# Optimization experiments

Hardware: AMD Instinct MI355X
Metric: run time of the kernel (lower is better)

Reference implementation:

```python
import jax, jax.numpy as jnp
import numpy as np
import math

# static configuration
SPATIAL_SHAPES = [(100, 150), (50, 75), (25, 38), (13, 19)]  # (H, W) per level
EMBED, HEADS, LEVELS, POINTS = 256, 8, 4, 4
HEAD_DIM = EMBED // HEADS
BS = 2
NV = sum(h * w for h, w in SPATIAL_SHAPES)  # 19947
NQ = NV  # encoder-style self-attention (value = query)


def _offset_bias():
    # replicate torch _init_weights grid init for sampling_offsets bias
    thetas = np.arange(HEADS, dtype=np.float32) * (2.0 * math.pi / HEADS)
    grid = np.stack([np.cos(thetas), np.sin(thetas)], -1)  # [H,2]
    grid = grid / np.abs(grid).max(-1, keepdims=True)
    grid = np.tile(grid[:, None, None, :], (1, LEVELS, POINTS, 1))
    for i in range(POINTS):
        grid[:, :, i, :] *= (i + 1)
    return jnp.asarray(grid.reshape(-1), dtype=jnp.float32)


def setup_inputs() -> dict:
    key = jax.random.key(0)
    ks = jax.random.split(key, 8)
    sc = 1.0 / math.sqrt(EMBED)
    return {
        "query": jax.random.normal(ks[0], (BS, NQ, EMBED), jnp.float32),
        "reference_points": jax.random.uniform(ks[1], (BS, NQ, LEVELS, 2), jnp.float32),
        "spatial_shapes": jnp.asarray(SPATIAL_SHAPES, dtype=jnp.int32),
        "W_off": jax.random.normal(ks[2], (EMBED, HEADS * LEVELS * POINTS * 2), jnp.float32) * 0.01,
        "b_off": _offset_bias(),
        "W_attn": jax.random.normal(ks[3], (EMBED, HEADS * LEVELS * POINTS), jnp.float32) * 0.01,
        "b_attn": jnp.zeros((HEADS * LEVELS * POINTS,), jnp.float32),
        "W_val": jax.random.normal(ks[4], (EMBED, EMBED), jnp.float32) * sc,
        "b_val": jnp.zeros((EMBED,), jnp.float32),
        "W_out": jax.random.normal(ks[5], (EMBED, EMBED), jnp.float32) * sc,
        "b_out": jnp.zeros((EMBED,), jnp.float32),
    }


def _bilinear_sample(value_l, loc_l, H, W):
    # value_l: [bs, H*W, heads, hd]; loc_l: [bs, nq, heads, P, 2] normalized coords
    # grid_sample semantics: align_corners=False, padding_mode='zeros'
    x = loc_l[..., 0] * W - 0.5
    y = loc_l[..., 1] * H - 0.5
    x0 = jnp.floor(x)
    y0 = jnp.floor(y)
    dx = x - x0
    dy = y - y0
    x0i = x0.astype(jnp.int32)
    y0i = y0.astype(jnp.int32)

    def gather(xi, yi):
        valid = (xi >= 0) & (xi < W) & (yi >= 0) & (yi < H)  # [bs,nq,h,P]
        idx = jnp.clip(yi, 0, H - 1) * W + jnp.clip(xi, 0, W - 1)
        bs, nq, h, P = idx.shape
        idx2 = idx.transpose(0, 1, 3, 2).reshape(bs, nq * P, h)[..., None]
        v = jnp.take_along_axis(value_l, idx2, axis=1)  # [bs, nq*P, h, hd]
        v = v.reshape(bs, nq, P, h, -1).transpose(0, 1, 3, 2, 4)  # [bs,nq,h,P,hd]
        return v * valid[..., None]

    w00 = ((1 - dx) * (1 - dy))[..., None]
    w01 = (dx * (1 - dy))[..., None]
    w10 = ((1 - dx) * dy)[..., None]
    w11 = (dx * dy)[..., None]
    return (gather(x0i, y0i) * w00 + gather(x0i + 1, y0i) * w01
            + gather(x0i, y0i + 1) * w10 + gather(x0i + 1, y0i + 1) * w11)


def reference(query, reference_points, spatial_shapes, W_off, b_off, W_attn, b_attn,
              W_val, b_val, W_out, b_out):
    bs, nq, _ = query.shape
    # value = query (encoder self-attn), identity = query
    value = (query @ W_val + b_val).reshape(bs, NV, HEADS, HEAD_DIM)
    offs = (query @ W_off + b_off).reshape(bs, nq, HEADS, LEVELS, POINTS, 2)
    attw = jax.nn.softmax((query @ W_attn + b_attn).reshape(bs, nq, HEADS, LEVELS * POINTS), axis=-1)
    attw = attw.reshape(bs, nq, HEADS, LEVELS, POINTS)
    # offset normalizer: (W, H) per level
    norm = jnp.stack([spatial_shapes[:, 1], spatial_shapes[:, 0]], -1).astype(query.dtype)
    loc = reference_points[:, :, None, :, None, :] + offs / norm[None, None, None, :, None, :]

    out = jnp.zeros((bs, nq, HEADS, HEAD_DIM), query.dtype)
    start = 0
    for lvl, (H, W) in enumerate(SPATIAL_SHAPES):
        value_l = value[:, start:start + H * W]  # static slice
        start += H * W
        sampled = _bilinear_sample(value_l, loc[:, :, :, lvl], H, W)  # [bs,nq,h,P,hd]
        out = out + jnp.einsum('bnhpc,bnhp->bnhc', sampled, attw[:, :, :, lvl, :])

    out = out.reshape(bs, nq, EMBED) @ W_out + b_out
    return out + query  # dropout(p=0) + identity
```

## Files before the change

kernel.cpp:

```cpp
#include <hip/hip_runtime.h>
#include <math.h>

#define HEADS     8
#define LEVELS    4
#define POINTS    4
#define HEAD_DIM  32
#define EMBED     256
#define NQ        19947
#define NV        19947
#define BS        2
#define M_ROWS    (BS * NQ)

typedef __bf16 bf16x8 __attribute__((ext_vector_type(8)));
typedef float  f32x4  __attribute__((ext_vector_type(4)));
typedef unsigned short ushort8 __attribute__((ext_vector_type(8)));

static __device__ __forceinline__ int lvl_H(int l) {
    constexpr int v[4] = {100, 50, 25, 13}; return v[l];
}
static __device__ __forceinline__ int lvl_W(int l) {
    constexpr int v[4] = {150, 75, 38, 19}; return v[l];
}
static __device__ __forceinline__ int lvl_start(int l) {
    constexpr int v[4] = {0, 15000, 18750, 19700}; return v[l];
}

static __device__ __forceinline__ unsigned short f2bf(float f) {
    unsigned u = __float_as_uint(f);
    u += 0x7fffu + ((u >> 16) & 1u);
    return (unsigned short)(u >> 16);
}

static __device__ __forceinline__ void gload_lds16(const void* g, void* l) {
    __builtin_amdgcn_global_load_lds(
        (const __attribute__((address_space(1))) void*)g,
        (__attribute__((address_space(3))) void*)l, 16, 0, 0);
}

static __device__ __forceinline__ void acc8(float* acc, uint4 u, float w) {
    acc[0] = fmaf(w, __uint_as_float(u.x << 16),        acc[0]);
    acc[1] = fmaf(w, __uint_as_float(u.x & 0xffff0000u), acc[1]);
    acc[2] = fmaf(w, __uint_as_float(u.y << 16),        acc[2]);
    acc[3] = fmaf(w, __uint_as_float(u.y & 0xffff0000u), acc[3]);
    acc[4] = fmaf(w, __uint_as_float(u.z << 16),        acc[4]);
    acc[5] = fmaf(w, __uint_as_float(u.z & 0xffff0000u), acc[5]);
    acc[6] = fmaf(w, __uint_as_float(u.w << 16),        acc[6]);
    acc[7] = fmaf(w, __uint_as_float(u.w & 0xffff0000u), acc[7]);
}

__global__ __launch_bounds__(256) void pack_query_kernel(
    const float* __restrict__ query, unsigned short* __restrict__ qbf)
{
    const int tid = blockIdx.x * 256 + threadIdx.x;
    if (tid >= M_ROWS * 32) return;
    const int row = tid >> 5;
    const int k8  = tid & 31;
    const float* src = query + (size_t)row * 256 + k8 * 8;
    const float4 v0 = *(const float4*)(src);
    const float4 v1 = *(const float4*)(src + 4);
    ushort8 o;
    o[0] = f2bf(v0.x); o[1] = f2bf(v0.y); o[2] = f2bf(v0.z); o[3] = f2bf(v0.w);
    o[4] = f2bf(v1.x); o[5] = f2bf(v1.y); o[6] = f2bf(v1.z); o[7] = f2bf(v1.w);
    const int g  = k8 >> 3;
    const int u2 = (k8 & 7) ^ (row & 7);
    *(ushort8*)((char*)qbf + (size_t)row * 512 + g * 128 + u2 * 16) = o;
}

__global__ __launch_bounds__(256) void pack_weights_kernel(
    const float* __restrict__ Wv, const float* __restrict__ Wo,
    const float* __restrict__ Wa, const float* __restrict__ Wout,
    unsigned short* __restrict__ Wcat, unsigned short* __restrict__ WoutT)
{
    const int tid = blockIdx.x * 256 + threadIdx.x;
    if (tid >= 896 * 32) return;
    const int row = tid >> 5;
    const int k8  = tid & 31;
    const float* src; int n_local, N; unsigned short* dstb; int r_local;
    if (row < 256)      { src = Wv;   n_local = row;       N = 256; dstb = Wcat;  r_local = row; }
    else if (row < 512) { src = Wo;   n_local = row - 256; N = 256; dstb = Wcat;  r_local = row; }
    else if (row < 640) { src = Wa;   n_local = row - 512; N = 128; dstb = Wcat;  r_local = row; }
    else                { src = Wout; n_local = row - 640; N = 256; dstb = WoutT; r_local = row - 640; }
    const int k = k8 * 8;
    ushort8 o;
    #pragma unroll
    for (int j = 0; j < 8; ++j)
        o[j] = f2bf(src[(size_t)(k + j) * N + n_local]);
    const int g  = k8 >> 3;
    const int u2 = (k8 & 7) ^ (r_local & 7);
    *(ushort8*)((char*)dstb + (size_t)r_local * 512 + g * 128 + u2 * 16) = o;
}

template <int EPI>
__global__ __launch_bounds__(256) void mfma_gemm_kernel(
    const unsigned short* __restrict__ Abf,
    const unsigned short* __restrict__ Bbf,
    unsigned short* __restrict__ value_bf,
    float* __restrict__ oa,
    const float* __restrict__ b_val, const float* __restrict__ b_off,
    const float* __restrict__ b_attn,
    const float* __restrict__ b_out, const float* __restrict__ query,
    float* __restrict__ out)
{
    __shared__ alignas(16) char As[16384];
    __shared__ alignas(16) char Bs[16384];

    const int t    = threadIdx.x;
    const int wid  = t >> 6;
    const int lane = t & 63;
    const int l15  = lane & 15;
    const int lhi  = lane >> 4;
    const int wr   = wid >> 1;
    const int wc   = wid & 1;
    const int m0   = blockIdx.x * 128;
    const int n0   = blockIdx.y * 128;

    f32x4 acc[4][4] = {};

    auto stage = [&](int ks) {
        #pragma unroll
        for (int j = 0; j < 4; ++j) {
            const int q  = j * 256 + wid * 64 + lane;
            const int tr = q >> 3;
            const int u  = q & 7;
            int gr = m0 + tr; gr = gr < M_ROWS ? gr : (M_ROWS - 1);
            gload_lds16((const char*)Abf + (size_t)gr * 512 + ks * 128 + u * 16,
                        As + (j * 256 + wid * 64) * 16);
            const int gn = n0 + tr;
            gload_lds16((const char*)Bbf + (size_t)gn * 512 + ks * 128 + u * 16,
                        Bs + (j * 256 + wid * 64) * 16);
        }
    };

    stage(0);
    for (int ks = 0; ks < 4; ++ks) {
        __syncthreads();
        #pragma unroll
        for (int kc = 0; kc < 2; ++kc) {
            bf16x8 a[4], b[4];
            #pragma unroll
            for (int i = 0; i < 4; ++i) {
                const int tr = wr * 64 + i * 16 + l15;
                const int ua = (kc * 4 + lhi) ^ (tr & 7);
                a[i] = *(const bf16x8*)&As[tr * 128 + ua * 16];
                const int tn = wc * 64 + i * 16 + l15;
                const int ub = (kc * 4 + lhi) ^ (tn & 7);
                b[i] = *(const bf16x8*)&Bs[tn * 128 + ub * 16];
            }
            #pragma unroll
            for (int i = 0; i < 4; ++i)
                #pragma unroll
                for (int j2 = 0; j2 < 4; ++j2)
                    acc[i][j2] = __builtin_amdgcn_mfma_f32_16x16x32_bf16(
                        a[i], b[j2], acc[i][j2], 0, 0, 0);
        }
        if (ks < 3) { __syncthreads(); stage(ks + 1); }
    }

    if (EPI == 0) {
        const int by = blockIdx.y;
        if (by < 2) {
            #pragma unroll
            for (int j2 = 0; j2 < 4; ++j2) {
                const int gn = n0 + wc * 64 + j2 * 16 + l15;
                const float bias = b_val[gn];
                const int h = gn >> 5, ch = gn & 31;
                #pragma unroll
                for (int i = 0; i < 4; ++i) {
                    #pragma unroll
                    for (int r = 0; r < 4; ++r) {
                        const int gm = m0 + wr * 64 + i * 16 + lhi * 4 + r;
                        if (gm >= M_ROWS) continue;
                        const int bb  = gm >= NQ;
                        const int pix = gm - bb * NQ;
                        value_bf[(((size_t)bb * 8 + h) * NV + pix) * 32 + ch] =
                            f2bf(acc[i][j2][r] + bias);
                    }
                }
            }
        } else {
            #pragma unroll
            for (int j2 = 0; j2 < 4; ++j2) {
                const int gn  = n0 + wc * 64 + j2 * 16 + l15;
                const int col = gn - 256;
                const float bias = (col < 256) ? b_off[col] : b_attn[col - 256];
                #pragma unroll
                for (int i = 0; i < 4; ++i) {
                    #pragma unroll
                    for (int r = 0; r < 4; ++r) {
                        const int gm = m0 + wr * 64 + i * 16 + lhi * 4 + r;
                        if (gm >= M_ROWS) continue;
                        oa[(size_t)gm * 384 + col] = acc[i][j2][r] + bias;
                    }
                }
            }
        }
    } else {
        #pragma unroll
        for (int j2 = 0; j2 < 4; ++j2) {
            const int gn = n0 + wc * 64 + j2 * 16 + l15;
            const float bias = b_out[gn];
            #pragma unroll
            for (int i = 0; i < 4; ++i) {
                #pragma unroll
                for (int r = 0; r < 4; ++r) {
                    const int gm = m0 + wr * 64 + i * 16 + lhi * 4 + r;
                    if (gm >= M_ROWS) continue;
                    out[(size_t)gm * 256 + gn] =
                        acc[i][j2][r] + bias + query[(size_t)gm * 256 + gn];
                }
            }
        }
    }
}

__global__ __launch_bounds__(256) void sample_kernel_v8(
    const unsigned short* __restrict__ value,
    const float* __restrict__ oa,
    const float* __restrict__ refp,
    unsigned short* __restrict__ outa_bf)
{
    __shared__ float4 cbuf[64][17];

    const int bx    = blockIdx.x;
    const int h     = bx & 7;
    const int chunk = bx >> 3;
    const int g     = threadIdx.x >> 2;
    const int q     = threadIdx.x & 3;
    const int row   = chunk * 64 + g;
    const bool valid = row < M_ROWS;

    if (valid) {
        const float* oar = oa + (size_t)row * 384;
        const float4 oxy0 = *(const float4*)(oar + h * 32 + q * 8);
        const float4 oxy1 = *(const float4*)(oar + h * 32 + q * 8 + 4);
        const float4 lgv  = *(const float4*)(oar + 256 + h * 16 + q * 4);

        float mx = fmaxf(fmaxf(lgv.x, lgv.y), fmaxf(lgv.z, lgv.w));
        mx = fmaxf(mx, __shfl_xor(mx, 1));
        mx = fmaxf(mx, __shfl_xor(mx, 2));
        const float e0 = expf(lgv.x - mx);
        const float e1 = expf(lgv.y - mx);
        const float e2 = expf(lgv.z - mx);
        const float e3 = expf(lgv.w - mx);
        float sum = e0 + e1 + e2 + e3;
        sum += __shfl_xor(sum, 1);
        sum += __shfl_xor(sum, 2);
        const float inv = 1.f / sum;

        const float2 rr = *(const float2*)(refp + (size_t)row * 8 + q * 2);
        const float rx = rr.x * (float)lvl_W(q) - 0.5f;
        const float ry = rr.y * (float)lvl_H(q) - 0.5f;

        cbuf[g][q * 4 + 0] = make_float4(oxy0.x + rx, oxy0.y + ry, e0 * inv, 0.f);
        cbuf[g][q * 4 + 1] = make_float4(oxy0.z + rx, oxy0.w + ry, e1 * inv, 0.f);
        cbuf[g][q * 4 + 2] = make_float4(oxy1.x + rx, oxy1.y + ry, e2 * inv, 0.f);
        cbuf[g][q * 4 + 3] = make_float4(oxy1.z + rx, oxy1.w + ry, e3 * inv, 0.f);
    }
    __syncthreads();
    if (!valid) return;

    const int b = row >= NQ;
    const unsigned short* vb = value + (((size_t)b * 8 + h) * NV) * 32 + q * 8;

    float acc[8] = {};
    #pragma unroll
    for (int l = 0; l < LEVELS; ++l) {
        const int W = lvl_W(l), H = lvl_H(l), st = lvl_start(l);
        #pragma unroll
        for (int p = 0; p < POINTS; ++p) {
            const float4 c = cbuf[g][l * 4 + p];
            const float fx = floorf(c.x), fy = floorf(c.y);
            const int x0 = (int)fx, y0 = (int)fy;
            const float dx = c.x - fx, dy = c.y - fy;
            const float omx = 1.f - dx, omy = 1.f - dy;
            float w00 = omx * omy * c.z;
            float w01 = dx  * omy * c.z;
            float w10 = omx * dy  * c.z;
            float w11 = dx  * dy  * c.z;
            const bool vx0 = (unsigned)x0       < (unsigned)W;
            const bool vx1 = (unsigned)(x0 + 1) < (unsigned)W;
            const bool vy0 = (unsigned)y0       < (unsigned)H;
            const bool vy1 = (unsigned)(y0 + 1) < (unsigned)H;
            w00 = (vx0 & vy0) ? w00 : 0.f;
            w01 = (vx1 & vy0) ? w01 : 0.f;
            w10 = (vx0 & vy1) ? w10 : 0.f;
            w11 = (vx1 & vy1) ? w11 : 0.f;
            const int xs0 = min(max(x0, 0), W - 1);
            const int xs1 = min(max(x0 + 1, 0), W - 1);
            const int ys0 = min(max(y0, 0), H - 1);
            const int ys1 = min(max(y0 + 1, 0), H - 1);
            const int r0i = st + ys0 * W;
            const int r1i = st + ys1 * W;
            const uint4 u00 = *(const uint4*)(vb + (size_t)(r0i + xs0) * 32);
            const uint4 u01 = *(const uint4*)(vb + (size_t)(r0i + xs1) * 32);
            const uint4 u10 = *(const uint4*)(vb + (size_t)(r1i + xs0) * 32);
            const uint4 u11 = *(const uint4*)(vb + (size_t)(r1i + xs1) * 32);
            acc8(acc, u00, w00);
            acc8(acc, u01, w01);
            acc8(acc, u10, w10);
            acc8(acc, u11, w11);
        }
    }

    unsigned d[4];
    #pragma unroll
    for (int i = 0; i < 4; ++i)
        d[i] = ((unsigned)f2bf(acc[2 * i + 1]) << 16) | (unsigned)f2bf(acc[2 * i]);
    const int bytecol = h * 64 + q * 16;
    const int g2 = bytecol >> 7;
    const int u2 = ((bytecol >> 4) & 7) ^ (row & 7);
    *(uint4*)((char*)outa_bf + (size_t)row * 512 + g2 * 128 + u2 * 16) = *(uint4*)d;
}

extern "C" void kernel_launch(void* const* d_in, const int* in_sizes, int n_in,
                              void* d_out, int out_size, void* d_ws, size_t ws_size,
                              hipStream_t stream)
{
    const float* query  = (const float*)d_in[0];
    const float* refp   = (const float*)d_in[1];
    const float* W_off  = (const float*)d_in[3];
    const float* b_off  = (const float*)d_in[4];
    const float* W_attn = (const float*)d_in[5];
    const float* b_attn = (const float*)d_in[6];
    const float* W_val  = (const float*)d_in[7];
    const float* b_val  = (const float*)d_in[8];
    const float* W_out  = (const float*)d_in[9];
    const float* b_out  = (const float*)d_in[10];
    float* out = (float*)d_out;

    char* p = (char*)d_ws;
    unsigned short* qbf   = (unsigned short*)p;
    unsigned short* oabf  = qbf;
    p += (size_t)M_ROWS * 512;
    unsigned short* value_bf = (unsigned short*)p;  p += (size_t)M_ROWS * 512;
    unsigned short* Wcat  = (unsigned short*)p;  p += (size_t)640 * 512;
    unsigned short* WoutT = (unsigned short*)p;  p += (size_t)256 * 512;
    float* oa = (float*)p;  p += (size_t)M_ROWS * 384 * 4;

    const dim3 blk(256);

    pack_query_kernel<<<(M_ROWS * 32 + 255) / 256, blk, 0, stream>>>(query, qbf);
    pack_weights_kernel<<<(896 * 32 + 255) / 256, blk, 0, stream>>>(
        W_val, W_off, W_attn, W_out, Wcat, WoutT);

    const dim3 g1((M_ROWS + 127) / 128, 5);
    mfma_gemm_kernel<0><<<g1, blk, 0, stream>>>(
        qbf, Wcat, value_bf, oa, b_val, b_off, b_attn,
        nullptr, nullptr, nullptr);

    const int chunks = (M_ROWS + 63) / 64;
    sample_kernel_v8<<<chunks * 8, blk, 0, stream>>>(value_bf, oa, refp, oabf);

    const dim3 g2((M_ROWS + 127) / 128, 2);
    mfma_gemm_kernel<1><<<g2, blk, 0, stream>>>(
        oabf, WoutT, nullptr, nullptr, nullptr, nullptr, nullptr,
        b_out, query, out);
}
```

Before: 169.4 us.

## Switch pipeline to fp16 and use packed half FMA with precomputed sample offsets

Converts all intermediate storage and the MFMA GEMMs from bf16 to fp16. The sampling kernel now accumulates with packed half2 FMAs instead of unpacking bf16 into fp32. Each thread now computes bilinear corner byte offsets and duplicated half weights for its level and writes them to LDS, so the gather loop only loads values and issues FMAs. The aim is to cut ALU work in the gather phase. The cost is lower accumulation precision (fp16 accumulation over 64 terms) and overflow risk from fp16's narrower range.

```diff
diff --git a/kernel.cpp b/kernel.cpp
--- a/kernel.cpp
+++ b/kernel.cpp
@@ -11,8 +11,9 @@
 #define BS        2
 #define M_ROWS    (BS * NQ)
 
-typedef __bf16 bf16x8 __attribute__((ext_vector_type(8)));
-typedef float  f32x4  __attribute__((ext_vector_type(4)));
+typedef _Float16 h8 __attribute__((ext_vector_type(8)));
+typedef _Float16 h2 __attribute__((ext_vector_type(2)));
+typedef float    f32x4 __attribute__((ext_vector_type(4)));
 typedef unsigned short ushort8 __attribute__((ext_vector_type(8)));
 
 static __device__ __forceinline__ int lvl_H(int l) {
@@ -25,10 +26,13 @@
     constexpr int v[4] = {0, 15000, 18750, 19700}; return v[l];
 }
 
-static __device__ __forceinline__ unsigned short f2bf(float f) {
-    unsigned u = __float_as_uint(f);
-    u += 0x7fffu + ((u >> 16) & 1u);
-    return (unsigned short)(u >> 16);
+static __device__ __forceinline__ unsigned short f2h(float f) {
+    _Float16 h = (_Float16)f;
+    return __builtin_bit_cast(unsigned short, h);
+}
+static __device__ __forceinline__ unsigned hdup(float w) {
+    const unsigned b = (unsigned)f2h(w);
+    return (b << 16) | b;
 }
 
 static __device__ __forceinline__ void gload_lds16(const void* g, void* l) {
@@ -37,19 +41,20 @@
         (__attribute__((address_space(3))) void*)l, 16, 0, 0);
 }
 
-static __device__ __forceinline__ void acc8(float* acc, uint4 u, float w) {
-    acc[0] = fmaf(w, __uint_as_float(u.x << 16),        acc[0]);
-    acc[1] = fmaf(w, __uint_as_float(u.x & 0xffff0000u), acc[1]);
-    acc[2] = fmaf(w, __uint_as_float(u.y << 16),        acc[2]);
-    acc[3] = fmaf(w, __uint_as_float(u.y & 0xffff0000u), acc[3]);
-    acc[4] = fmaf(w, __uint_as_float(u.z << 16),        acc[4]);
-    acc[5] = fmaf(w, __uint_as_float(u.z & 0xffff0000u), acc[5]);
-    acc[6] = fmaf(w, __uint_as_float(u.w << 16),        acc[6]);
-    acc[7] = fmaf(w, __uint_as_float(u.w & 0xffff0000u), acc[7]);
+static __device__ __forceinline__ void pkacc(h2* acc, uint4 u, unsigned wbits) {
+    const h2 w = __builtin_bit_cast(h2, wbits);
+    h2 v0 = __builtin_bit_cast(h2, u.x);
+    h2 v1 = __builtin_bit_cast(h2, u.y);
+    h2 v2 = __builtin_bit_cast(h2, u.z);
+    h2 v3 = __builtin_bit_cast(h2, u.w);
+    acc[0] = v0 * w + acc[0];
+    acc[1] = v1 * w + acc[1];
+    acc[2] = v2 * w + acc[2];
+    acc[3] = v3 * w + acc[3];
 }
 
 __global__ __launch_bounds__(256) void pack_query_kernel(
-    const float* __restrict__ query, unsigned short* __restrict__ qbf)
+    const float* __restrict__ query, unsigned short* __restrict__ qh)
 {
     const int tid = blockIdx.x * 256 + threadIdx.x;
     if (tid >= M_ROWS * 32) return;
@@ -59,11 +64,11 @@
     const float4 v0 = *(const float4*)(src);
     const float4 v1 = *(const float4*)(src + 4);
     ushort8 o;
-    o[0] = f2bf(v0.x); o[1] = f2bf(v0.y); o[2] = f2bf(v0.z); o[3] = f2bf(v0.w);
-    o[4] = f2bf(v1.x); o[5] = f2bf(v1.y); o[6] = f2bf(v1.z); o[7] = f2bf(v1.w);
+    o[0] = f2h(v0.x); o[1] = f2h(v0.y); o[2] = f2h(v0.z); o[3] = f2h(v0.w);
+    o[4] = f2h(v1.x); o[5] = f2h(v1.y); o[6] = f2h(v1.z); o[7] = f2h(v1.w);
     const int g  = k8 >> 3;
     const int u2 = (k8 & 7) ^ (row & 7);
-    *(ushort8*)((char*)qbf + (size_t)row * 512 + g * 128 + u2 * 16) = o;
+    *(ushort8*)((char*)qh + (size_t)row * 512 + g * 128 + u2 * 16) = o;
 }
 
 __global__ __launch_bounds__(256) void pack_weights_kernel(
@@ -84,7 +89,7 @@
     ushort8 o;
     #pragma unroll
     for (int j = 0; j < 8; ++j)
-        o[j] = f2bf(src[(size_t)(k + j) * N + n_local]);
+        o[j] = f2h(src[(size_t)(k + j) * N + n_local]);
     const int g  = k8 >> 3;
     const int u2 = (k8 & 7) ^ (r_local & 7);
     *(ushort8*)((char*)dstb + (size_t)r_local * 512 + g * 128 + u2 * 16) = o;
@@ -92,9 +97,9 @@
 
 template <int EPI>
 __global__ __launch_bounds__(256) void mfma_gemm_kernel(
-    const unsigned short* __restrict__ Abf,
-    const unsigned short* __restrict__ Bbf,
-    unsigned short* __restrict__ value_bf,
+    const unsigned short* __restrict__ Ah,
+    const unsigned short* __restrict__ Bh,
+    unsigned short* __restrict__ value_h,
     float* __restrict__ oa,
     const float* __restrict__ b_val, const float* __restrict__ b_off,
     const float* __restrict__ b_attn,
@@ -123,10 +128,10 @@
             const int tr = q >> 3;
             const int u  = q & 7;
             int gr = m0 + tr; gr = gr < M_ROWS ? gr : (M_ROWS - 1);
-            gload_lds16((const char*)Abf + (size_t)gr * 512 + ks * 128 + u * 16,
+            gload_lds16((const char*)Ah + (size_t)gr * 512 + ks * 128 + u * 16,
                         As + (j * 256 + wid * 64) * 16);
             const int gn = n0 + tr;
-            gload_lds16((const char*)Bbf + (size_t)gn * 512 + ks * 128 + u * 16,
+            gload_lds16((const char*)Bh + (size_t)gn * 512 + ks * 128 + u * 16,
                         Bs + (j * 256 + wid * 64) * 16);
         }
     };
@@ -136,21 +141,21 @@
         __syncthreads();
         #pragma unroll
         for (int kc = 0; kc < 2; ++kc) {
-            bf16x8 a[4], b[4];
+            h8 a[4], b[4];
             #pragma unroll
             for (int i = 0; i < 4; ++i) {
                 const int tr = wr * 64 + i * 16 + l15;
                 const int ua = (kc * 4 + lhi) ^ (tr & 7);
-                a[i] = *(const bf16x8*)&As[tr * 128 + ua * 16];
+                a[i] = *(const h8*)&As[tr * 128 + ua * 16];
                 const int tn = wc * 64 + i * 16 + l15;
                 const int ub = (kc * 4 + lhi) ^ (tn & 7);
-                b[i] = *(const bf16x8*)&Bs[tn * 128 + ub * 16];
+                b[i] = *(const h8*)&Bs[tn * 128 + ub * 16];
             }
             #pragma unroll
             for (int i = 0; i < 4; ++i)
                 #pragma unroll
                 for (int j2 = 0; j2 < 4; ++j2)
-                    acc[i][j2] = __builtin_amdgcn_mfma_f32_16x16x32_bf16(
+                    acc[i][j2] = __builtin_amdgcn_mfma_f32_16x16x32_f16(
                         a[i], b[j2], acc[i][j2], 0, 0, 0);
         }
         if (ks < 3) { __syncthreads(); stage(ks + 1); }
@@ -172,8 +177,8 @@
                         if (gm >= M_ROWS) continue;
                         const int bb  = gm >= NQ;
                         const int pix = gm - bb * NQ;
-                        value_bf[(((size_t)bb * 8 + h) * NV + pix) * 32 + ch] =
-                            f2bf(acc[i][j2][r] + bias);
+                        value_h[(((size_t)bb * 8 + h) * NV + pix) * 32 + ch] =
+                            f2h(acc[i][j2][r] + bias);
                     }
                 }
             }
@@ -213,13 +218,14 @@
     }
 }
 
-__global__ __launch_bounds__(256) void sample_kernel_v8(
+__global__ __launch_bounds__(256) void sample_kernel_v9(
     const unsigned short* __restrict__ value,
     const float* __restrict__ oa,
     const float* __restrict__ refp,
-    unsigned short* __restrict__ outa_bf)
-{
-    __shared__ float4 cbuf[64][17];
+    unsigned short* __restrict__ outa_h)
+{
+    __shared__ uint4 offs_lds[16][64];
+    __shared__ uint4 w_lds[16][64];
 
     const int bx    = blockIdx.x;
     const int h     = bx & 7;
@@ -230,10 +236,11 @@
     const bool valid = row < M_ROWS;
 
     if (valid) {
+        const int lvl = q;
         const float* oar = oa + (size_t)row * 384;
-        const float4 oxy0 = *(const float4*)(oar + h * 32 + q * 8);
-        const float4 oxy1 = *(const float4*)(oar + h * 32 + q * 8 + 4);
-        const float4 lgv  = *(const float4*)(oar + 256 + h * 16 + q * 4);
+        const float4 oxy0 = *(const float4*)(oar + h * 32 + lvl * 8);
+        const float4 oxy1 = *(const float4*)(oar + h * 32 + lvl * 8 + 4);
+        const float4 lgv  = *(const float4*)(oar + 256 + h * 16 + lvl * 4);
 
         float mx = fmaxf(fmaxf(lgv.x, lgv.y), fmaxf(lgv.z, lgv.w));
         mx = fmaxf(mx, __shfl_xor(mx, 1));
@@ -247,36 +254,26 @@
         sum += __shfl_xor(sum, 2);
         const float inv = 1.f / sum;
 
-        const float2 rr = *(const float2*)(refp + (size_t)row * 8 + q * 2);
-        const float rx = rr.x * (float)lvl_W(q) - 0.5f;
-        const float ry = rr.y * (float)lvl_H(q) - 0.5f;
-
-        cbuf[g][q * 4 + 0] = make_float4(oxy0.x + rx, oxy0.y + ry, e0 * inv, 0.f);
-        cbuf[g][q * 4 + 1] = make_float4(oxy0.z + rx, oxy0.w + ry, e1 * inv, 0.f);
-        cbuf[g][q * 4 + 2] = make_float4(oxy1.x + rx, oxy1.y + ry, e2 * inv, 0.f);
-        cbuf[g][q * 4 + 3] = make_float4(oxy1.z + rx, oxy1.w + ry, e3 * inv, 0.f);
-    }
-    __syncthreads();
-    if (!valid) return;
-
-    const int b = row >= NQ;
-    const unsigned short* vb = value + (((size_t)b * 8 + h) * NV) * 32 + q * 8;
-
-    float acc[8] = {};
-    #pragma unroll
-    for (int l = 0; l < LEVELS; ++l) {
-        const int W = lvl_W(l), H = lvl_H(l), st = lvl_start(l);
+        const float2 rr = *(const float2*)(refp + (size_t)row * 8 + lvl * 2);
+        const int W = lvl_W(lvl), H = lvl_H(lvl), st = lvl_start(lvl);
+        const float rx = rr.x * (float)W - 0.5f;
+        const float ry = rr.y * (float)H - 0.5f;
+
+        const float sxv[4] = {oxy0.x + rx, oxy0.z + rx, oxy1.x + rx, oxy1.z + rx};
+        const float syv[4] = {oxy0.y + ry, oxy0.w + ry, oxy1.y + ry, oxy1.w + ry};
+        const float ev[4]  = {e0 * inv, e1 * inv, e2 * inv, e3 * inv};
+
         #pragma unroll
-        for (int p = 0; p < POINTS; ++p) {
-            const float4 c = cbuf[g][l * 4 + p];
-            const float fx = floorf(c.x), fy = floorf(c.y);
+        for (int p = 0; p < 4; ++p) {
+            const float cx = sxv[p], cy = syv[p], wz = ev[p];
+            const float fx = floorf(cx), fy = floorf(cy);
             const int x0 = (int)fx, y0 = (int)fy;
-            const float dx = c.x - fx, dy = c.y - fy;
+            const float dx = cx - fx, dy = cy - fy;
             const float omx = 1.f - dx, omy = 1.f - dy;
-            float w00 = omx * omy * c.z;
-            float w01 = dx  * omy * c.z;
-            float w10 = omx * dy  * c.z;
-            float w11 = dx  * dy  * c.z;
+            float w00 = omx * omy * wz;
+            float w01 = dx  * omy * wz;
+            float w10 = omx * dy  * wz;
+            float w11 = dx  * dy  * wz;
             const bool vx0 = (unsigned)x0       < (unsigned)W;
             const bool vx1 = (unsigned)(x0 + 1) < (unsigned)W;
             const bool vy0 = (unsigned)y0       < (unsigned)H;
@@ -291,25 +288,43 @@
             const int ys1 = min(max(y0 + 1, 0), H - 1);
             const int r0i = st + ys0 * W;
             const int r1i = st + ys1 * W;
-            const uint4 u00 = *(const uint4*)(vb + (size_t)(r0i + xs0) * 32);
-            const uint4 u01 = *(const uint4*)(vb + (size_t)(r0i + xs1) * 32);
-            const uint4 u10 = *(const uint4*)(vb + (size_t)(r1i + xs0) * 32);
-            const uint4 u11 = *(const uint4*)(vb + (size_t)(r1i + xs1) * 32);
-            acc8(acc, u00, w00);
-            acc8(acc, u01, w01);
-            acc8(acc, u10, w10);
-            acc8(acc, u11, w11);
+            uint4 off;
+            off.x = (unsigned)(r0i + xs0) * 64u;
+            off.y = (unsigned)(r0i + xs1) * 64u;
+            off.z = (unsigned)(r1i + xs0) * 64u;
+            off.w = (unsigned)(r1i + xs1) * 64u;
+            uint4 wv;
+            wv.x = hdup(w00); wv.y = hdup(w01); wv.z = hdup(w10); wv.w = hdup(w11);
+            offs_lds[lvl * 4 + p][g] = off;
+            w_lds[lvl * 4 + p][g]    = wv;
         }
     }
-
-    unsigned d[4];
+    __syncthreads();
+    if (!valid) return;
+
+    const int b = row >= NQ;
+    const char* vb = (const char*)(value + (((size_t)b * 8 + h) * NV) * 32 + q * 8);
+
+    h2 acc[4] = {};
     #pragma unroll
-    for (int i = 0; i < 4; ++i)
-        d[i] = ((unsigned)f2bf(acc[2 * i + 1]) << 16) | (unsigned)f2bf(acc[2 * i]);
+    for (int s = 0; s < 16; ++s) {
+        const uint4 off = offs_lds[s][g];
+        const uint4 wv  = w_lds[s][g];
+        const uint4 u00 = *(const uint4*)(vb + off.x);
+        const uint4 u01 = *(const uint4*)(vb + off.y);
+        const uint4 u10 = *(const uint4*)(vb + off.z);
+        const uint4 u11 = *(const uint4*)(vb + off.w);
+        pkacc(acc, u00, wv.x);
+        pkacc(acc, u01, wv.y);
+        pkacc(acc, u10, wv.z);
+        pkacc(acc, u11, wv.w);
+    }
+
     const int bytecol = h * 64 + q * 16;
     const int g2 = bytecol >> 7;
     const int u2 = ((bytecol >> 4) & 7) ^ (row & 7);
-    *(uint4*)((char*)outa_bf + (size_t)row * 512 + g2 * 128 + u2 * 16) = *(uint4*)d;
+    *(uint4*)((char*)outa_h + (size_t)row * 512 + g2 * 128 + u2 * 16) =
+        *(const uint4*)acc;
 }
 
 extern "C" void kernel_launch(void* const* d_in, const int* in_sizes, int n_in,
@@ -329,30 +344,30 @@
     float* out = (float*)d_out;
 
     char* p = (char*)d_ws;
-    unsigned short* qbf   = (unsigned short*)p;
-    unsigned short* oabf  = qbf;
+    unsigned short* qh    = (unsigned short*)p;
+    unsigned short* oah   = qh;
     p += (size_t)M_ROWS * 512;
-    unsigned short* value_bf = (unsigned short*)p;  p += (size_t)M_ROWS * 512;
+    unsigned short* value_h = (unsigned short*)p;  p += (size_t)M_ROWS * 512;
     unsigned short* Wcat  = (unsigned short*)p;  p += (size_t)640 * 512;
     unsigned short* WoutT = (unsigned short*)p;  p += (size_t)256 * 512;
     float* oa = (float*)p;  p += (size_t)M_ROWS * 384 * 4;
 
     const dim3 blk(256);
 
-    pack_query_kernel<<<(M_ROWS * 32 + 255) / 256, blk, 0, stream>>>(query, qbf);
+    pack_query_kernel<<<(M_ROWS * 32 + 255) / 256, blk, 0, stream>>>(query, qh);
     pack_weights_kernel<<<(896 * 32 + 255) / 256, blk, 0, stream>>>(
         W_val, W_off, W_attn, W_out, Wcat, WoutT);
 
     const dim3 g1((M_ROWS + 127) / 128, 5);
     mfma_gemm_kernel<0><<<g1, blk, 0, stream>>>(
-        qbf, Wcat, value_bf, oa, b_val, b_off, b_attn,
+        qh, Wcat, value_h, oa, b_val, b_off, b_attn,
         nullptr, nullptr, nullptr);
 
     const int chunks = (M_ROWS + 63) / 64;
-    sample_kernel_v8<<<chunks * 8, blk, 0, stream>>>(value_bf, oa, refp, oabf);
+    sample_kernel_v9<<<chunks * 8, blk, 0, stream>>>(value_h, oa, refp, oah);
 
     const dim3 g2((M_ROWS + 127) / 128, 2);
     mfma_gemm_kernel<1><<<g2, blk, 0, stream>>>(
-        oabf, WoutT, nullptr, nullptr, nullptr, nullptr, nullptr,
+        oah, WoutT, nullptr, nullptr, nullptr, nullptr, nullptr,
         b_out, query, out);
 }
```

Measured after the change: 160.9 us. -5.0%, faster.
